# Optimization experiments

Measured on AMD Instinct MI355X. Metric: run time of the kernel, lower is better.

## Reference

```python
import jax, jax.numpy as jnp
import numpy as np

K = 9          # kernel_size
CENTER = K // 2
EXTEND = 1.0   # extend_scope
B, C_IN, C_OUT, H, W = 2, 64, 64, 256, 256


def group_norm(x, w, b, groups, eps=1e-5):
    Bx, C, Hx, Wx = x.shape
    xg = x.reshape(Bx, groups, C // groups, Hx, Wx)
    m = xg.mean(axis=(2, 3, 4), keepdims=True)
    v = xg.var(axis=(2, 3, 4), keepdims=True)
    xn = ((xg - m) * jax.lax.rsqrt(v + eps)).reshape(Bx, C, Hx, Wx)
    return xn * w[None, :, None, None] + b[None, :, None, None]


def conv2d(x, w, b, stride, padding):
    y = jax.lax.conv_general_dilated(x, w, stride, padding,
                                     dimension_numbers=('NCHW', 'OIHW', 'NCHW'))
    return y + b[None, :, None, None]


def bilinear_sample(feat, iy, ix):
    # feat [B,C,H,W]; iy/ix pixel coords [B,Hg,Wg]; align_corners=True bilinear
    Hf, Wf = feat.shape[2], feat.shape[3]
    y0 = jnp.floor(iy); x0 = jnp.floor(ix)
    wy1 = iy - y0; wx1 = ix - x0
    wy0 = 1.0 - wy1; wx0 = 1.0 - wx1
    y0i = jnp.clip(y0, 0, Hf - 1).astype(jnp.int32)
    y1i = jnp.clip(y0 + 1, 0, Hf - 1).astype(jnp.int32)
    x0i = jnp.clip(x0, 0, Wf - 1).astype(jnp.int32)
    x1i = jnp.clip(x0 + 1, 0, Wf - 1).astype(jnp.int32)
    g = jax.vmap(lambda f, yi, xi: f[:, yi, xi])  # per-batch gather -> [B,C,Hg,Wg]
    return (g(feat, y0i, x0i) * (wy0 * wx0)[:, None]
            + g(feat, y0i, x1i) * (wy0 * wx1)[:, None]
            + g(feat, y1i, x0i) * (wy1 * wx0)[:, None]
            + g(feat, y1i, x1i) * (wy1 * wx1)[:, None])


def outward_cumsum(off):
    # off [B,K,H,W]: center row -> 0, cumulative sums outward from center
    lower = jnp.flip(jnp.cumsum(jnp.flip(off[:, :CENTER], axis=1), axis=1), axis=1)
    upper = jnp.cumsum(off[:, CENTER + 1:], axis=1)
    zero = jnp.zeros_like(off[:, :1])
    return jnp.concatenate([lower, zero, upper], axis=1)


def reference(x, w_off, b_off, gno_w, gno_b, w_dsc, b_dsc, gn_w, gn_b):
    Bx, _, Hx, Wx = x.shape
    # offset branch: conv3x3 -> GroupNorm(K, 2K) -> tanh
    offset = conv2d(x, w_off, b_off, (1, 1), ((1, 1), (1, 1)))
    offset = jnp.tanh(group_norm(offset, gno_w, gno_b, groups=K))
    y_off = offset[:, :K]                      # morph=0 uses the y half
    y_cum = outward_cumsum(y_off)              # [B,K,H,W]
    y_center = jnp.arange(Hx, dtype=x.dtype)[None, None, :, None]
    x_base = (jnp.arange(Wx, dtype=x.dtype)[None, None, None, :]
              + jnp.linspace(-CENTER, CENTER, K, dtype=x.dtype)[None, :, None, None])
    y_new = y_center + EXTEND * y_cum          # [B,K,H,W]
    x_new = jnp.broadcast_to(x_base, y_new.shape)
    # permute(0,2,1,3).reshape -> [B, K*H, W]
    ycoord = y_new.transpose(0, 2, 1, 3).reshape(Bx, Hx * K, Wx)
    xcoord = x_new.transpose(0, 2, 1, 3).reshape(Bx, Hx * K, Wx)
    # clamp to [0,max] then [-1,1] normalize + align_corners unnormalize == clamp
    iy = jnp.clip(ycoord, 0.0, Hx - 1.0)
    ix = jnp.clip(xcoord, 0.0, Wx - 1.0)
    deformed = bilinear_sample(x, iy, ix)      # [B,C,K*H,W]
    out = conv2d(deformed, w_dsc, b_dsc, (K, 1), 'VALID')  # [B,Cout,H,W]
    out = group_norm(out, gn_w, gn_b, groups=C_OUT // 4)
    return jax.nn.relu(out)


def setup_inputs() -> dict:
    key = jax.random.key(0)
    ks = jax.random.split(key, 3)
    return {
        'x': jax.random.normal(ks[0], (B, C_IN, H, W), dtype=jnp.float32),
        'w_off': jax.random.normal(ks[1], (2 * K, C_IN, 3, 3), dtype=jnp.float32) * 0.05,
        'b_off': jnp.zeros((2 * K,), dtype=jnp.float32),
        'gno_w': jnp.ones((2 * K,), dtype=jnp.float32),
        'gno_b': jnp.zeros((2 * K,), dtype=jnp.float32),
        'w_dsc': jax.random.normal(ks[2], (C_OUT, C_IN, K, 1), dtype=jnp.float32) * 0.05,
        'b_dsc': jnp.zeros((C_OUT,), dtype=jnp.float32),
        'gn_w': jnp.ones((C_OUT,), dtype=jnp.float32),
        'gn_b': jnp.zeros((C_OUT,), dtype=jnp.float32),
    }
```

## Files before the change

### kernel.cpp

```cpp
#include <hip/hip_runtime.h>
#include <hip/hip_fp16.h>
#include <math.h>

#define BB 2
#define CC 64
#define HH 256
#define WW 256
#define KK 9
#define NOFF 10
#define HW (HH*WW)

typedef __attribute__((ext_vector_type(8))) short s16x8;
typedef __attribute__((ext_vector_type(4))) float f32x4;

__device__ __forceinline__ unsigned lerp2h(unsigned a, unsigned b, __half2 fy2) {
    __half2 ah = *(__half2*)&a, bh = *(__half2*)&b;
    __half2 d = __hfma2(fy2, __hsub2(bh, ah), ah);
    return *(unsigned*)&d;
}

__device__ __forceinline__ float fast_tanh(float z) {
    float e = __builtin_amdgcn_exp2f(z * 2.885390081777927f);
    return 1.f - 2.f * __builtin_amdgcn_rcpf(e + 1.f);
}

__device__ __forceinline__ void swizzle_bhw(int g, int& b, int& h, int& wt) {
    int W = ((g & 7) << 8) | (g >> 3);
    b  = W >> 10;
    int rem = W & 1023;
    h  = rem >> 2;
    wt = rem & 3;
}




__global__ __launch_bounds__(256) void transpose_x_kernel(const float* __restrict__ x,
                                                          unsigned short* __restrict__ xTh,
                                                          const float* __restrict__ w_off,
                                                          const float* __restrict__ w_dsc,
                                                          unsigned short* __restrict__ woffB,
                                                          unsigned short* __restrict__ wdscB,
                                                          float* __restrict__ sums_off,
                                                          float* __restrict__ sums_out) {
    if (blockIdx.x >= 2048) {
        int idx = (blockIdx.x - 2048) * 256 + threadIdx.x;
        if (blockIdx.x == 2048) {
            int t = threadIdx.x;
            for (int i = t; i < 128 * 32; i += 256) sums_off[i] = 0.f;
            for (int i = t; i < 128 * 32; i += 256) sums_out[i] = 0.f;
        }
        if (idx < 18 * 64 * 8) {
            int kb = idx >> 9;
            int L  = (idx >> 3) & 63;
            int j  = idx & 7;
            int n = L & 15, quad = L >> 4;
            int kk = kb * 32 + quad * 8 + j;
            int tap = kk >> 6, ci = kk & 63;
            float v = (n < NOFF) ? w_off[(n * 64 + ci) * 9 + tap] : 0.f;
            __half hv = __float2half(v);
            woffB[idx] = *(unsigned short*)&hv;
        }
        if (idx < 4 * 18 * 64 * 8) {
            int nt = idx / 9216;
            int r  = idx - nt * 9216;
            int kb = r >> 9;
            int L  = (r >> 3) & 63;
            int j  = r & 7;
            int n = L & 15, quad = L >> 4;
            int co = nt * 16 + n;
            int kk = kb * 32 + quad * 8 + j;
            int k = kk >> 6, ci = kk & 63;
            __half hv = __float2half(w_dsc[(co * 64 + ci) * 9 + k]);
            wdscB[idx] = *(unsigned short*)&hv;
        }
        return;
    }
    __shared__ float tile[64 * 65];
    int wt = blockIdx.x & 3;
    int h  = (blockIdx.x >> 2) & 255;
    int b  = blockIdx.x >> 10;
    int w0 = wt * 64;
    int t  = threadIdx.x;
    {
        int wq = t & 15, c0 = t >> 4;
#pragma unroll
        for (int it = 0; it < 4; ++it) {
            int c = c0 + it * 16;
            float4 v = *(const float4*)&x[(((b * CC + c) * HH + h) * WW) + w0 + wq * 4];
            tile[(wq * 4 + 0) * 65 + c] = v.x;
            tile[(wq * 4 + 1) * 65 + c] = v.y;
            tile[(wq * 4 + 2) * 65 + c] = v.z;
            tile[(wq * 4 + 3) * 65 + c] = v.w;
        }
    }
    __syncthreads();
    {
        int c8 = t & 7, wr = t >> 3;
        uint4* dst = (uint4*)xTh;
#pragma unroll
        for (int it = 0; it < 2; ++it) {
            int wl = wr + it * 32;
            const float* row = &tile[wl * 65 + c8 * 8];
            __half2 p0 = __floats2half2_rn(row[0], row[1]);
            __half2 p1 = __floats2half2_rn(row[2], row[3]);
            __half2 p2 = __floats2half2_rn(row[4], row[5]);
            __half2 p3 = __floats2half2_rn(row[6], row[7]);
            uint4 d;
            d.x = *(unsigned*)&p0; d.y = *(unsigned*)&p1;
            d.z = *(unsigned*)&p2; d.w = *(unsigned*)&p3;
            dst[((size_t)((b * HH + h) * WW) + w0 + wl) * 8 + c8] = d;
        }
    }
}

#define CPITCH 72
__global__ __launch_bounds__(256) void conv_off_mfma(const unsigned short* __restrict__ xTh,
                                                     const unsigned short* __restrict__ woffB,
                                                     const float* __restrict__ b_off,
                                                     unsigned short* __restrict__ off_raw,
                                                     float* __restrict__ sums_off) {
    __shared__ unsigned short sx[3 * 66 * CPITCH];
    __shared__ float rs[4][16], rs2[4][16];
    int t = threadIdx.x;
    int L = t & 63, v = t >> 6;
    int b, h, wt;
    swizzle_bhw(blockIdx.x, b, h, wt);
    int w0 = wt << 6;
    int col = L & 15, quad = L >> 4;

#pragma unroll
    for (int it = 0; it < 7; ++it) {
        int linear = it * 256 + t;
        if (linear < 1584) {
            int dy  = linear / 528;
            int rem = linear - dy * 528;
            int px  = rem >> 3, cg = rem & 7;
            int y  = h - 1 + dy;
            int xc = w0 - 1 + px;
            uint4 d = make_uint4(0, 0, 0, 0);
            if ((unsigned)y < 256u && (unsigned)xc < 256u)
                d = *(const uint4*)(xTh + ((size_t)(((b << 8) + y) << 8) + xc) * 64 + cg * 8);
            *(uint4*)&sx[(dy * 66 + px) * CPITCH + cg * 8] = d;
        }
    }

    s16x8 breg[18];
#pragma unroll
    for (int kb = 0; kb < 18; ++kb)
        breg[kb] = *(const s16x8*)(woffB + (kb * 64 + L) * 8);
    __syncthreads();

    f32x4 acc = {0.f, 0.f, 0.f, 0.f};
    __builtin_amdgcn_s_setprio(1);
#pragma unroll
    for (int kb = 0; kb < 18; ++kb) {
        int tap = kb >> 1;
        int dy = tap / 3, dxl = tap % 3;
        int pxl = v * 16 + col + dxl;
        int ci0 = ((kb & 1) << 5) + quad * 8;
        s16x8 a = *(const s16x8*)&sx[(dy * 66 + pxl) * CPITCH + ci0];
        acc = __builtin_amdgcn_mfma_f32_16x16x32_f16(a, breg[kb], acc, 0, 0, 0);
    }
    __builtin_amdgcn_s_setprio(0);
    int oc = col;
    float bo = b_off[oc];
    float s = 0.f, s2 = 0.f;
#pragma unroll
    for (int r = 0; r < 4; ++r) {
        float val = acc[r] + bo;
        if (oc < NOFF) {
            int w = w0 + v * 16 + quad * 4 + r;
            __half hv = __float2half(val);
            off_raw[((b * NOFF + oc) << 16) + (h << 8) + w] = *(unsigned short*)&hv;
        }
        s += val; s2 += val * val;
    }
    s  += __shfl_xor(s, 16, 64);  s  += __shfl_xor(s, 32, 64);
    s2 += __shfl_xor(s2, 16, 64); s2 += __shfl_xor(s2, 32, 64);
    if (quad == 0) { rs[v][oc] = s; rs2[v][oc] = s2; }
    __syncthreads();
    if (t < NOFF) {
        float a_ = rs[0][t] + rs[1][t] + rs[2][t] + rs[3][t];
        float a2 = rs2[0][t] + rs2[1][t] + rs2[2][t] + rs2[3][t];
        float* dst = sums_off + ((b << 6) + (blockIdx.x & 63)) * 32 + (t >> 1) * 2;
        atomicAdd(&dst[0], a_);
        atomicAdd(&dst[1], a2);
    }
}

__global__ __launch_bounds__(256) void main_mfma(const unsigned short* __restrict__ xTh,
                                                 const unsigned short* __restrict__ off_raw,
                                                 const float* __restrict__ sums_off,
                                                 const float* __restrict__ gno_w,
                                                 const float* __restrict__ gno_b,
                                                 const unsigned short* __restrict__ wdscB,
                                                 const float* __restrict__ b_dsc,
                                                 unsigned short* __restrict__ tmph,
                                                 float* __restrict__ sums_out) {
    __shared__ unsigned short aT[16 * 584];
    __shared__ unsigned       offs[576];
    __shared__ unsigned short fys[576];

    int t = threadIdx.x;
    int L = t & 63, nt = t >> 6;
    int b, h, wt;
    swizzle_bhw(blockIdx.x, b, h, wt);
    int w0 = wt << 6;
    int bBase = b << 22;

    if (t < 64) {
        float sv[10];
        const float* p = sums_off + ((b << 6) + t) * 32;
#pragma unroll
        for (int i = 0; i < 10; ++i) sv[i] = p[i];
#pragma unroll
        for (int o = 1; o <= 32; o <<= 1) {
#pragma unroll
            for (int i = 0; i < 10; ++i) sv[i] += __shfl_xor(sv[i], o, 64);
        }
        float msg[5], rsg[5];
#pragma unroll
        for (int g = 0; g < 5; ++g) {
            float mean = sv[g * 2] * (1.f / 131072.f);
            float var  = sv[g * 2 + 1] * (1.f / 131072.f) - mean * mean;
            msg[g] = mean;
            rsg[g] = rsqrtf(var + 1e-5f);
        }
        int w = w0 + t;
        float tk[9];
#pragma unroll
        for (int k = 0; k < 9; ++k) {
            unsigned short u = off_raw[((b * NOFF + k) << 16) + (h << 8) + w];
            float vv = __half2float(*(__half*)&u);
            int g = k >> 1;
            tk[k] = fast_tanh((vv - msg[g]) * rsg[g] * gno_w[k] + gno_b[k]);
        }
        float yc[9];
        float c = 0.f;
#pragma unroll
        for (int k = 3; k >= 0; --k) { c += tk[k]; yc[k] = c; }
        yc[4] = 0.f;
        c = 0.f;
#pragma unroll
        for (int k = 5; k < 9; ++k) { c += tk[k]; yc[k] = c; }
#pragma unroll
        for (int k = 0; k < 9; ++k) {
            float y = fminf(fmaxf((float)h + yc[k], 0.f), 255.f);
            float y0f = floorf(y);
            int y0 = (int)y0f;
            int xc = min(max(w + k - 4, 0), 255);
            __half fh = __float2half(y - y0f);
            offs[t * 9 + k] = (unsigned)(bBase + (y0 << 14) + (xc << 6));
            fys[t * 9 + k]  = *(unsigned short*)&fh;
        }
    }

    s16x8 wreg[18];
#pragma unroll
    for (int kb = 0; kb < 18; ++kb)
        wreg[kb] = *(const s16x8*)(wdscB + ((nt * 18 + kb) * 64 + L) * 8);

    int col = L & 15, quad = L >> 4;
    int co = nt * 16 + col;
    float bias = b_dsc[co];
    float ss = 0.f, ss2 = 0.f;

    for (int round = 0; round < 4; ++round) {
        __syncthreads();
#pragma unroll
        for (int it = 0; it < 5; ++it) {
            int idx = it * 256 + t;
            if (idx < 1152) {
                int cg  = idx & 7;
                int r2  = idx >> 3;
                int pxl = r2 / 9;
                int k   = r2 - pxl * 9;
                int pi  = (round * 16 + pxl) * 9 + k;
                unsigned o0 = offs[pi] + (cg << 3);
                unsigned short fb = fys[pi];
                unsigned o1 = fb ? o0 + 16384 : o0;
                __half fh = *(__half*)&fb;
                __half2 fy2 = __half2half2(fh);
                uint4 u0 = *(const uint4*)(xTh + o0);
                uint4 u1 = *(const uint4*)(xTh + o1);
                uint4 d;
                d.x = lerp2h(u0.x, u1.x, fy2);
                d.y = lerp2h(u0.y, u1.y, fy2);
                d.z = lerp2h(u0.z, u1.z, fy2);
                d.w = lerp2h(u0.w, u1.w, fy2);
                int c2 = (cg + k) & 7;
                *(uint4*)&aT[pxl * 584 + k * 64 + c2 * 8] = d;
            }
        }
        __syncthreads();

        {
            int row = col;
            f32x4 acc = {0.f, 0.f, 0.f, 0.f};
            __builtin_amdgcn_s_setprio(1);
#pragma unroll
            for (int kb = 0; kb < 18; ++kb) {
                int k  = kb >> 1;
                int cch = ((kb & 1) << 2) + quad;
                int c2 = (cch + k) & 7;
                s16x8 a = *(const s16x8*)&aT[row * 584 + k * 64 + c2 * 8];
                acc = __builtin_amdgcn_mfma_f32_16x16x32_f16(a, wreg[kb], acc, 0, 0, 0);
            }
            __builtin_amdgcn_s_setprio(0);
            int wblk = (w0 >> 2) + round * 4 + quad;
            size_t ebase = ((size_t)(((b << 8) + h) << 6) + wblk) * 64 + co;
            float v0 = acc[0] + bias, v1 = acc[1] + bias;
            float v2 = acc[2] + bias, v3 = acc[3] + bias;
            ss  += v0 + v1 + v2 + v3;
            ss2 += v0 * v0 + v1 * v1 + v2 * v2 + v3 * v3;
            __half2 p0 = __floats2half2_rn(v0, v1);
            __half2 p1 = __floats2half2_rn(v2, v3);
            uint2 pk;
            pk.x = *(unsigned*)&p0;
            pk.y = *(unsigned*)&p1;
            ((uint2*)tmph)[ebase] = pk;
        }
    }
    ss  += __shfl_xor(ss, 16, 64);  ss  += __shfl_xor(ss, 32, 64);
    ss2 += __shfl_xor(ss2, 16, 64); ss2 += __shfl_xor(ss2, 32, 64);
    float sg = ss, sg2 = ss2;
    sg  += __shfl_xor(sg, 1, 64);  sg  += __shfl_xor(sg, 2, 64);
    sg2 += __shfl_xor(sg2, 1, 64); sg2 += __shfl_xor(sg2, 2, 64);
    if (quad == 0 && (col & 3) == 0) {
        int gi = nt * 4 + (col >> 2);
        float* dst = sums_out + ((b << 6) + (blockIdx.x & 63)) * 32 + gi * 2;
        atomicAdd(&dst[0], sg);
        atomicAdd(&dst[1], sg2);
    }
}

__global__ __launch_bounds__(256) void apply_final_kernel(const unsigned short* __restrict__ tmph,
                                                          const float* __restrict__ sums_out,
                                                          const float* __restrict__ gn_w,
                                                          const float* __restrict__ gn_b,
                                                          float* __restrict__ out) {
    __shared__ float tile[64 * 65];
    __shared__ float statsS[32];
    int wt = blockIdx.x & 3;
    int h  = (blockIdx.x >> 2) & 255;
    int b  = blockIdx.x >> 10;
    int w0 = wt * 64;
    int t  = threadIdx.x;
    {
        int i8 = t >> 3, sb = t & 7;
        float s = 0.f;
#pragma unroll
        for (int bk = sb; bk < 64; bk += 8)
            s += sums_out[((b << 6) + bk) * 32 + i8];
        s += __shfl_xor(s, 1, 64); s += __shfl_xor(s, 2, 64); s += __shfl_xor(s, 4, 64);
        if (sb == 0) statsS[i8] = s;
    }
    __syncthreads();
    {
        int co = t & 63, wb0 = t >> 6;
        int g = co >> 2;
        float s0 = statsS[g * 2], s1 = statsS[g * 2 + 1];
        float mean = s0 * (1.f / 262144.f);
        float var  = s1 * (1.f / 262144.f) - mean * mean;
        float rstd = rsqrtf(var + 1e-5f);
        float sc = rstd * gn_w[co];
        float sh = gn_b[co] - mean * sc;
        const uint2* src = (const uint2*)tmph;
#pragma unroll
        for (int it = 0; it < 4; ++it) {
            int wb = wb0 + it * 4;
            size_t bp = (size_t)(((b << 8) + h) << 6) + (w0 >> 2) + wb;
            uint2 u = src[bp * 64 + co];
            float2 f0 = __half22float2(*(__half2*)&u.x);
            float2 f1 = __half22float2(*(__half2*)&u.y);
            float* dst = &tile[co * 65 + wb * 4];
            dst[0] = fmaxf(fmaf(f0.x, sc, sh), 0.f);
            dst[1] = fmaxf(fmaf(f0.y, sc, sh), 0.f);
            dst[2] = fmaxf(fmaf(f1.x, sc, sh), 0.f);
            dst[3] = fmaxf(fmaf(f1.y, sc, sh), 0.f);
        }
    }
    __syncthreads();
    {
        int wq = t & 15, c0 = t >> 4;
#pragma unroll
        for (int it = 0; it < 4; ++it) {
            int co = c0 + it * 16;
            const float* row = &tile[co * 65 + wq * 4];
            float4 v;
            v.x = row[0]; v.y = row[1]; v.z = row[2]; v.w = row[3];
            *(float4*)&out[((size_t)(b * CC + co) * HH + h) * WW + w0 + wq * 4] = v;
        }
    }
}

extern "C" void kernel_launch(void* const* d_in, const int* in_sizes, int n_in,
                              void* d_out, int out_size, void* d_ws, size_t ws_size,
                              hipStream_t stream) {
    const float* x     = (const float*)d_in[0];
    const float* w_off = (const float*)d_in[1];
    const float* b_off = (const float*)d_in[2];
    const float* gno_w = (const float*)d_in[3];
    const float* gno_b = (const float*)d_in[4];
    const float* w_dsc = (const float*)d_in[5];
    const float* b_dsc = (const float*)d_in[6];
    const float* gn_w  = (const float*)d_in[7];
    const float* gn_b  = (const float*)d_in[8];
    float* out = (float*)d_out;

    char* ws = (char*)d_ws;
    unsigned short* xTh     = (unsigned short*)(ws);
    unsigned short* tmph    = (unsigned short*)(ws + 16777216);
    unsigned short* off_raw = (unsigned short*)(ws + 33554432);
    unsigned short* wdscB   = (unsigned short*)(ws + 36175872);
    unsigned short* woffB   = (unsigned short*)(ws + 36249600);
    float* sums_off         = (float*)(ws + 36268032);
    float* sums_out         = (float*)(ws + 36284416);

    hipLaunchKernelGGL(transpose_x_kernel, dim3(2192), dim3(256), 0, stream,
                       x, xTh, w_off, w_dsc, woffB, wdscB, sums_off, sums_out);
    hipLaunchKernelGGL(conv_off_mfma, dim3(2048), dim3(256), 0, stream,
                       xTh, woffB, b_off, off_raw, sums_off);
    hipLaunchKernelGGL(main_mfma, dim3(2048), dim3(256), 0, stream,
                       xTh, off_raw, sums_off, gno_w, gno_b, wdscB, b_dsc,
                       tmph, sums_out);
    hipLaunchKernelGGL(apply_final_kernel, dim3(2048), dim3(256), 0, stream,
                       tmph, sums_out, gn_w, gn_b, out);
}
```

Measured before the change: 155.8 us.

## Software-pipeline bilinear gathers with MFMA compute across rounds

```diff
diff --git a/kernel.cpp b/kernel.cpp
--- a/kernel.cpp
+++ b/kernel.cpp
@@ -31,7 +31,6 @@
     h  = rem >> 2;
     wt = rem & 3;
 }
-
 
 
 
@@ -199,8 +198,7 @@
                                                  unsigned short* __restrict__ tmph,
                                                  float* __restrict__ sums_out) {
     __shared__ unsigned short aT[16 * 584];
-    __shared__ unsigned       offs[576];
-    __shared__ unsigned short fys[576];
+    __shared__ uint2 coordP[576];
 
     int t = threadIdx.x;
     int L = t & 63, nt = t >> 6;
@@ -251,8 +249,8 @@
             int y0 = (int)y0f;
             int xc = min(max(w + k - 4, 0), 255);
             __half fh = __float2half(y - y0f);
-            offs[t * 9 + k] = (unsigned)(bBase + (y0 << 14) + (xc << 6));
-            fys[t * 9 + k]  = *(unsigned short*)&fh;
+            coordP[t * 9 + k] = make_uint2((unsigned)(bBase + (y0 << 14) + (xc << 6)),
+                                           (unsigned)(*(unsigned short*)&fh));
         }
     }
 
@@ -266,34 +264,56 @@
     float bias = b_dsc[co];
     float ss = 0.f, ss2 = 0.f;
 
-    for (int round = 0; round < 4; ++round) {
-        __syncthreads();
+    int tt = t >> 3, cg = t & 7;
+    int r2a[5], wadr[5];
+#pragma unroll
+    for (int it = 0; it < 5; ++it) {
+        int r2 = it * 32 + tt;
+        r2a[it] = r2;
+        int pxl = r2 / 9, k = r2 - pxl * 9;
+        wadr[it] = pxl * 584 + k * 64 + (((cg + k) & 7) << 3);
+    }
+
+    uint2 rc[5];
+    uint4 u0[5], u1[5];
+
+    auto issue = [&](int rr) {
 #pragma unroll
         for (int it = 0; it < 5; ++it) {
-            int idx = it * 256 + t;
-            if (idx < 1152) {
-                int cg  = idx & 7;
-                int r2  = idx >> 3;
-                int pxl = r2 / 9;
-                int k   = r2 - pxl * 9;
-                int pi  = (round * 16 + pxl) * 9 + k;
-                unsigned o0 = offs[pi] + (cg << 3);
-                unsigned short fb = fys[pi];
-                unsigned o1 = fb ? o0 + 16384 : o0;
+            if (it < 4 || t < 128) {
+                uint2 c2v = coordP[rr * 144 + r2a[it]];
+                rc[it] = c2v;
+                unsigned o0 = c2v.x + (cg << 3);
+                unsigned o1 = c2v.y ? o0 + 16384 : o0;
+                u0[it] = *(const uint4*)(xTh + o0);
+                u1[it] = *(const uint4*)(xTh + o1);
+            }
+        }
+    };
+    auto consume = [&]() {
+#pragma unroll
+        for (int it = 0; it < 5; ++it) {
+            if (it < 4 || t < 128) {
+                unsigned short fb = (unsigned short)rc[it].y;
                 __half fh = *(__half*)&fb;
                 __half2 fy2 = __half2half2(fh);
-                uint4 u0 = *(const uint4*)(xTh + o0);
-                uint4 u1 = *(const uint4*)(xTh + o1);
                 uint4 d;
-                d.x = lerp2h(u0.x, u1.x, fy2);
-                d.y = lerp2h(u0.y, u1.y, fy2);
-                d.z = lerp2h(u0.z, u1.z, fy2);
-                d.w = lerp2h(u0.w, u1.w, fy2);
-                int c2 = (cg + k) & 7;
-                *(uint4*)&aT[pxl * 584 + k * 64 + c2 * 8] = d;
+                d.x = lerp2h(u0[it].x, u1[it].x, fy2);
+                d.y = lerp2h(u0[it].y, u1[it].y, fy2);
+                d.z = lerp2h(u0[it].z, u1[it].z, fy2);
+                d.w = lerp2h(u0[it].w, u1[it].w, fy2);
+                *(uint4*)&aT[wadr[it]] = d;
             }
         }
+    };
+
+    __syncthreads();
+    issue(0);
+
+    for (int r = 0; r < 4; ++r) {
+        consume();
         __syncthreads();
+        if (r < 3) issue(r + 1);
 
         {
             int row = col;
@@ -308,7 +328,7 @@
                 acc = __builtin_amdgcn_mfma_f32_16x16x32_f16(a, wreg[kb], acc, 0, 0, 0);
             }
             __builtin_amdgcn_s_setprio(0);
-            int wblk = (w0 >> 2) + round * 4 + quad;
+            int wblk = (w0 >> 2) + r * 4 + quad;
             size_t ebase = ((size_t)(((b << 8) + h) << 6) + wblk) * 64 + co;
             float v0 = acc[0] + bias, v1 = acc[1] + bias;
             float v2 = acc[2] + bias, v3 = acc[3] + bias;
@@ -321,6 +341,7 @@
             pk.y = *(unsigned*)&p1;
             ((uint2*)tmph)[ebase] = pk;
         }
+        if (r < 3) __syncthreads();
     }
     ss  += __shfl_xor(ss, 16, 64);  ss  += __shfl_xor(ss, 32, 64);
     ss2 += __shfl_xor(ss2, 16, 64); ss2 += __shfl_xor(ss2, 32, 64);
```

After: 147.2 us. 1.06x faster.
